# Kernel optimization log

Hardware: AMD Instinct MI355X
Metric: run time of the kernel (lower is better)

Reference implementation:

```python
import jax, jax.numpy as jnp
import numpy as np

N, K, C = 2, 512, 256
IMG = 1024.0
P = 7            # output_size
S = 2            # sampling_ratio
SCALES = (0.25, 0.125, 0.0625, 0.03125)
MIN_LEVEL, MAX_LEVEL = 2, 5
CANON_SIZE, CANON_LEVEL = 224.0, 4


def setup_inputs() -> dict:
    key = jax.random.key(0)
    ks = jax.random.split(key, 7)
    feats = {}
    for i, (hw, kk) in enumerate(zip((256, 128, 64, 32), ks[:4])):
        feats[f"feat{i + 2}"] = jax.random.normal(kk, (N, C, hw, hw), dtype=jnp.float32)
    # boxes: centers uniform in image, sizes log-uniform in [32, 512] px -> spans all levels
    cxy = jax.random.uniform(ks[4], (N, K, 2), minval=0.0, maxval=IMG)
    wh = 32.0 * jnp.exp2(jax.random.uniform(ks[5], (N, K, 2), minval=0.0, maxval=4.0))
    x1y1 = jnp.clip(cxy - wh / 2, 0.0, IMG)
    x2y2 = jnp.clip(cxy + wh / 2, 0.0, IMG)
    boxes = jnp.concatenate([x1y1, x2y2], axis=-1).astype(jnp.float32)  # [N,K,4] xyxy
    feats["boxes"] = boxes
    return feats


def _roi_align_level(feat, boxes, batch_idx, scale):
    """ROIAlignV2 (aligned=True). feat [N,C,H,W], boxes [M,4] xyxy in image coords."""
    Nf, Cf, H, W = feat.shape
    M = boxes.shape[0]
    b = boxes * scale - 0.5  # aligned=True shift
    x1, y1, x2, y2 = b[:, 0], b[:, 1], b[:, 2], b[:, 3]
    bin_h = (y2 - y1) / P
    bin_w = (x2 - x1) / P
    # combined bin+sample grid: coord = start + ((i + 0.5)/S) * bin, i in [0, P*S)
    g = (jnp.arange(P * S, dtype=feat.dtype) + 0.5) / S  # [PS]
    y = y1[:, None] + g[None, :] * bin_h[:, None]  # [M, PS]
    x = x1[:, None] + g[None, :] * bin_w[:, None]  # [M, PS]

    def prep(c, size):
        valid = (c >= -1.0) & (c <= size)
        c = jnp.maximum(c, 0.0)
        lo = jnp.minimum(jnp.floor(c).astype(jnp.int32), size - 1)
        hi = jnp.minimum(lo + 1, size - 1)
        frac = c - lo.astype(c.dtype)  # harmless if >1 when lo==hi==size-1
        return lo, hi, frac, valid

    yl, yh, fy, vy = prep(y, H)
    xl, xh, fx, vx = prep(x, W)
    bi = batch_idx[:, None, None]

    def gather(yy, xx):
        # -> [M, PS, PS, C]
        return feat[bi, :, yy[:, :, None], xx[:, None, :]]

    fy_ = fy[:, :, None, None]
    fx_ = fx[:, None, :, None]
    v = ((1 - fy_) * ((1 - fx_) * gather(yl, xl) + fx_ * gather(yl, xh))
         + fy_ * ((1 - fx_) * gather(yh, xl) + fx_ * gather(yh, xh)))
    mask = (vy[:, :, None] & vx[:, None, :])[..., None]
    v = jnp.where(mask, v, jnp.zeros((), feat.dtype))
    out = v.reshape(M, P, S, P, S, Cf).mean(axis=(2, 4))  # avg over sampling grid
    return out.transpose(0, 3, 1, 2)  # [M, C, P, P]


def reference(feat2, feat3, feat4, feat5, boxes):
    feats = [feat2, feat3, feat4, feat5]
    flat = boxes.reshape(-1, 4)  # [M,4], concat over images
    batch_idx = jnp.repeat(jnp.arange(N, dtype=jnp.int32), K)
    # assign_boxes_to_levels
    area = (flat[:, 2] - flat[:, 0]) * (flat[:, 3] - flat[:, 1])
    sizes = jnp.sqrt(area)
    lvl = jnp.floor(CANON_LEVEL + jnp.log2(sizes / CANON_SIZE + 1e-8))
    lvl = jnp.clip(lvl, MIN_LEVEL, MAX_LEVEL).astype(jnp.int32) - MIN_LEVEL  # [M] in 0..3
    out = jnp.zeros((flat.shape[0], C, P, P), dtype=feat2.dtype)
    for l, (feat, scale) in enumerate(zip(feats, SCALES)):
        o = _roi_align_level(feat, flat, batch_idx, scale)
        out = jnp.where((lvl == l)[:, None, None, None], o, out)
    return out
```

## Files before the change

kernel.cpp:

```cpp
#include <hip/hip_runtime.h>
#include <hip/hip_fp16.h>
#include <math.h>
#include <stdint.h>

#define NBATCH 2
#define KBOX   512
#define NBOX   (NBATCH*KBOX)
#define CCH    256
#define NBIN   49
#define NCH    4
#define BPB    (CCH/NCH)
#define COUT   (CCH*NBIN)
#define WCAP   1280
#define HDRN   32
#define TAPN   (12*NBIN)

typedef const uint32_t __attribute__((address_space(1)))* gas_u32p;
typedef uint32_t       __attribute__((address_space(3)))* las_u32p;

__global__ __launch_bounds__(64) void box_prep_kernel(
    const float* __restrict__ boxes, int* __restrict__ hdr, uint32_t* __restrict__ taps)
{
    const int m    = blockIdx.x;
    const int lane = threadIdx.x;

    __shared__ float    s_fy[14], s_fx[14];
    __shared__ int      s_slo[14], s_shi[14], s_xr[14];
    __shared__ int      s_vy[14], s_vx[14];
    __shared__ int      s_wsp4;
    __shared__ uint16_t s_roff[28];

    const float x1 = boxes[m*4+0];
    const float y1 = boxes[m*4+1];
    const float x2 = boxes[m*4+2];
    const float y2 = boxes[m*4+3];

    const float area = (x2 - x1) * (y2 - y1);
    const float size = sqrtf(area);
    float lvlf = floorf(4.0f + log2f(size / 224.0f + 1e-8f));
    lvlf = fminf(fmaxf(lvlf, 2.0f), 5.0f);
    const int lvl = (int)lvlf - 2;

    const int   H     = 256 >> lvl;
    const float scale = 0.25f / (float)(1 << lvl);
    const float Hf    = (float)H;

    const float bx1 = x1 * scale - 0.5f;
    const float by1 = y1 * scale - 0.5f;
    const float bin_w = (x2 * scale - 0.5f - bx1) / 7.0f;
    const float bin_h = (y2 * scale - 0.5f - by1) / 7.0f;

    if (lane == 0) {
        int xls[14];
        #pragma unroll 1
        for (int i = 0; i < 14; ++i) {
            const float gx = ((float)i + 0.5f) * 0.5f;
            const float xx = bx1 + gx * bin_w;
            s_vx[i] = (xx >= -1.0f) && (xx <= Hf);
            const float xc = fmaxf(xx, 0.0f);
            const int xl = min((int)floorf(xc), H - 1);
            const int xh = min(xl + 1, H - 1);
            float fx = xc - (float)xl;
            if (xh == xl) fx = 0.0f;
            s_fx[i] = fx;
            xls[i] = xl;
        }
        const int wx0a = xls[0] & ~3;
        const int xh13 = min(xls[13] + 1, H - 1);
        const int wsp4 = ((xh13 - wx0a + 1 + 3) >> 2) << 2;
        s_wsp4 = wsp4;
        #pragma unroll 1
        for (int i = 0; i < 14; ++i) s_xr[i] = xls[i] - wx0a;

        unsigned long long bm[4] = {0ull, 0ull, 0ull, 0ull};
        int yls[14], yhs[14];
        #pragma unroll 1
        for (int j = 0; j < 14; ++j) {
            const float gy = ((float)j + 0.5f) * 0.5f;
            const float yy = by1 + gy * bin_h;
            s_vy[j] = (yy >= -1.0f) && (yy <= Hf);
            const float yc = fmaxf(yy, 0.0f);
            const int yl = min((int)floorf(yc), H - 1);
            const int yh = min(yl + 1, H - 1);
            s_fy[j] = yc - (float)yl;
            yls[j] = yl; yhs[j] = yh;
            bm[yl >> 6] |= 1ull << (yl & 63);
            bm[yh >> 6] |= 1ull << (yh & 63);
        }
        int cum[4];
        cum[0] = 0;
        cum[1] = cum[0] + (int)__popcll(bm[0]);
        cum[2] = cum[1] + (int)__popcll(bm[1]);
        cum[3] = cum[2] + (int)__popcll(bm[2]);
        const int nr = cum[3] + (int)__popcll(bm[3]);
        #pragma unroll 1
        for (int j = 0; j < 14; ++j) {
            const int yl = yls[j], yh = yhs[j];
            s_slo[j] = cum[yl >> 6] + (int)__popcll(bm[yl >> 6] & ((1ull << (yl & 63)) - 1ull));
            s_shi[j] = cum[yh >> 6] + (int)__popcll(bm[yh >> 6] & ((1ull << (yh & 63)) - 1ull));
        }
        int slot = 0;
        #pragma unroll 1
        for (int w = 0; w < 4; ++w) {
            unsigned long long t = bm[w];
            while (t) {
                const int b = __builtin_ctzll(t);
                t &= t - 1ull;
                s_roff[slot++] = (uint16_t)(((w << 6) + b) * H + wx0a);
            }
        }
        #pragma unroll 1
        for (int r = slot; r < 28; ++r) s_roff[r] = s_roff[slot - 1];

        int* h = hdr + m * HDRN;
        const int qpr = wsp4 >> 2;
        const int nq  = nr * qpr;
        h[0] = lvl;
        h[1] = H;
        h[2] = H * H;
        h[3] = qpr;
        h[4] = nq;
        h[5] = __float_as_int(1.0f / (float)qpr);
        h[6] = nq << 2;
        h[7] = 0;
        uint32_t* hw = (uint32_t*)(h + 8);
        #pragma unroll 1
        for (int k = 0; k < 14; ++k)
            hw[k] = (uint32_t)s_roff[2*k] | ((uint32_t)s_roff[2*k+1] << 16);
    }
    __syncthreads();

    if (lane < NBIN) {
        const int py = lane / 7;
        const int px = lane - py * 7;
        const uint32_t base = (uint32_t)m * TAPN;
        __half2* th = (__half2*)taps;
        const int wsp4 = s_wsp4;

        #pragma unroll
        for (int s = 0; s < 4; ++s) {
            const int j = 2*py + (s >> 1);
            const int i = 2*px + (s & 1);
            const float fy = s_fy[j];
            const float fx = s_fx[i];
            const float vm = (s_vy[j] && s_vx[i]) ? 0.25f : 0.0f;
            const float wyl = (1.0f - fy) * vm;
            const float wyh = fy * vm;

            const uint32_t olo = (uint32_t)(s_slo[j] * wsp4 + s_xr[i]);
            const uint32_t ohi = (uint32_t)(s_shi[j] * wsp4 + s_xr[i]);

            taps[base + s*NBIN + lane] = olo | (ohi << 16);
            th  [base + (4+s)*NBIN + lane] = __floats2half2_rn(wyl*(1.0f-fx), wyh*(1.0f-fx));
            th  [base + (8+s)*NBIN + lane] = __floats2half2_rn(wyl*fx,        wyh*fx);
        }
    }
}

__global__ __launch_bounds__(256, 8) void roi_align_kernel(
    const float* __restrict__ f2, const float* __restrict__ f3,
    const float* __restrict__ f4, const float* __restrict__ f5,
    const int* __restrict__ hdr, const uint32_t* __restrict__ taps,
    float* __restrict__ out)
{
    const int bid  = blockIdx.x;
    const int m    = bid >> 6;
    const int cg   = bid & 63;
    const int tid  = threadIdx.x;
    const int lane = tid & 63;
    const int wid  = tid >> 6;
    const int b    = m >> 9;

    __shared__ float win[NCH * WCAP];

    const int* h = hdr + m * HDRN;
    const int   lvl = h[0];
    const int   HH  = h[2];
    const int   qpr = h[3];
    const int   nq  = h[4];
    const float rq  = __int_as_float(h[5]);
    const int   nq4 = h[6];

    const uint32_t roww = ((const uint32_t*)(h + 8))[min(lane, 13)];

    const float* fptr = (lvl == 0) ? f2 : (lvl == 1) ? f3 : (lvl == 2) ? f4 : f5;
    const int c = cg * NCH + wid;
    const float* plane = fptr + ((size_t)(b * CCH + c)) * HH;
    float* wbase = win + wid * WCAP;

    const int niter = (nq + 63) >> 6;
    for (int it = 0; it < niter; ++it) {
        const int iq  = (it << 6) + lane;
        const int iqc = min(iq, nq - 1);
        const int slot = (int)(((float)iqc + 0.5f) * rq);
        const int cq   = iqc - slot * qpr;
        const uint32_t w2 = (uint32_t)__shfl((int)roww, slot >> 1, 64);
        const int roff = (slot & 1) ? (int)(w2 >> 16) : (int)(w2 & 0xffffu);
        if (iq < nq) {
            __builtin_amdgcn_global_load_lds(
                (gas_u32p)(const void*)(plane + roff + (cq << 2)),
                (las_u32p)(void*)(&wbase[it << 8]),
                16, 0, 0);
        }
    }
    if (lane == 0) wbase[nq4] = 0.0f;

    const int l = (lane < NBIN) ? lane : NBIN - 1;
    const uint32_t* tb = taps + (uint32_t)m * TAPN;
    const __half2*  th = (const __half2*)tb;

    uint32_t po[4];
    __half2  wl[4], wh[4];
    #pragma unroll
    for (int s = 0; s < 4; ++s) po[s] = tb[s*NBIN + l];
    #pragma unroll
    for (int s = 0; s < 4; ++s) wl[s] = th[(4+s)*NBIN + l];
    #pragma unroll
    for (int s = 0; s < 4; ++s) wh[s] = th[(8+s)*NBIN + l];

    asm volatile("s_waitcnt vmcnt(0) lgkmcnt(0)" ::: "memory");
    __builtin_amdgcn_sched_barrier(0);

    float acc = 0.0f;
    #pragma unroll
    for (int s = 0; s < 4; ++s) {
        const int olo = (int)(po[s] & 0xffffu);
        const int ohi = (int)(po[s] >> 16);
        const float2 a  = __half22float2(wl[s]);
        const float2 bw = __half22float2(wh[s]);
        acc += a.x * wbase[olo] + bw.x * wbase[olo + 1];
        acc += a.y * wbase[ohi] + bw.y * wbase[ohi + 1];
    }

    if (lane < NBIN) {
        __builtin_nontemporal_store(
            acc, out + (size_t)m * COUT + (size_t)c * NBIN + lane);
    }
}

extern "C" void kernel_launch(void* const* d_in, const int* in_sizes, int n_in,
                              void* d_out, int out_size, void* d_ws, size_t ws_size,
                              hipStream_t stream) {
    const float* f2    = (const float*)d_in[0];
    const float* f3    = (const float*)d_in[1];
    const float* f4    = (const float*)d_in[2];
    const float* f5    = (const float*)d_in[3];
    const float* boxes = (const float*)d_in[4];
    float* outp = (float*)d_out;

    int*      hdr  = (int*)d_ws;
    uint32_t* taps = (uint32_t*)d_ws + NBOX * HDRN;

    box_prep_kernel<<<dim3(NBOX), dim3(64), 0, stream>>>(boxes, hdr, taps);
    roi_align_kernel<<<dim3(NBOX * BPB), dim3(256), 0, stream>>>(
        f2, f3, f4, f5, hdr, taps, outp);
}
```

Baseline: 110.3 us.

## Process two channels per wave and interleave tap records for vector loads

Each wave now handles two channels, so the tap offsets and weights it loads and the index math it does are shared across both channels. The grid shrinks to half the blocks. Tap data is stored interleaved per bin so each lane fetches its 12 words with three 16-byte vector loads instead of twelve strided scalar loads. The LDS window per channel is reduced to 1024 floats, which keeps total shared memory similar, and the occupancy hint drops to 5. The costs are lower parallelism, more registers per thread, and a risk of overflowing the window if a box needs more than 1024 floats.

```diff
diff --git a/kernel.cpp b/kernel.cpp
--- a/kernel.cpp
+++ b/kernel.cpp
@@ -8,10 +8,12 @@
 #define NBOX   (NBATCH*KBOX)
 #define CCH    256
 #define NBIN   49
-#define NCH    4
-#define BPB    (CCH/NCH)
+#define CPW    2
+#define WAVES  4
+#define CHB    (CPW*WAVES)
+#define BPB    (CCH/CHB)
 #define COUT   (CCH*NBIN)
-#define WCAP   1280
+#define WCAP   1024
 #define HDRN   32
 #define TAPN   (12*NBIN)
 
@@ -133,8 +135,7 @@
     if (lane < NBIN) {
         const int py = lane / 7;
         const int px = lane - py * 7;
-        const uint32_t base = (uint32_t)m * TAPN;
-        __half2* th = (__half2*)taps;
+        uint32_t* tp = taps + ((uint32_t)m * NBIN + lane) * 12u;
         const int wsp4 = s_wsp4;
 
         #pragma unroll
@@ -150,28 +151,31 @@
             const uint32_t olo = (uint32_t)(s_slo[j] * wsp4 + s_xr[i]);
             const uint32_t ohi = (uint32_t)(s_shi[j] * wsp4 + s_xr[i]);
 
-            taps[base + s*NBIN + lane] = olo | (ohi << 16);
-            th  [base + (4+s)*NBIN + lane] = __floats2half2_rn(wyl*(1.0f-fx), wyh*(1.0f-fx));
-            th  [base + (8+s)*NBIN + lane] = __floats2half2_rn(wyl*fx,        wyh*fx);
+            const __half2 wlo2 = __floats2half2_rn(wyl*(1.0f-fx), wyh*(1.0f-fx));
+            const __half2 whi2 = __floats2half2_rn(wyl*fx,        wyh*fx);
+
+            tp[s]     = olo | (ohi << 16);
+            tp[4 + s] = *reinterpret_cast<const uint32_t*>(&wlo2);
+            tp[8 + s] = *reinterpret_cast<const uint32_t*>(&whi2);
         }
     }
 }
 
-__global__ __launch_bounds__(256, 8) void roi_align_kernel(
+__global__ __launch_bounds__(256, 5) void roi_align_kernel(
     const float* __restrict__ f2, const float* __restrict__ f3,
     const float* __restrict__ f4, const float* __restrict__ f5,
     const int* __restrict__ hdr, const uint32_t* __restrict__ taps,
     float* __restrict__ out)
 {
     const int bid  = blockIdx.x;
-    const int m    = bid >> 6;
-    const int cg   = bid & 63;
+    const int m    = bid >> 5;
+    const int cg   = bid & 31;
     const int tid  = threadIdx.x;
     const int lane = tid & 63;
     const int wid  = tid >> 6;
     const int b    = m >> 9;
 
-    __shared__ float win[NCH * WCAP];
+    __shared__ float win[WAVES * CPW * WCAP];
 
     const int* h = hdr + m * HDRN;
     const int   lvl = h[0];
@@ -184,9 +188,11 @@
     const uint32_t roww = ((const uint32_t*)(h + 8))[min(lane, 13)];
 
     const float* fptr = (lvl == 0) ? f2 : (lvl == 1) ? f3 : (lvl == 2) ? f4 : f5;
-    const int c = cg * NCH + wid;
-    const float* plane = fptr + ((size_t)(b * CCH + c)) * HH;
-    float* wbase = win + wid * WCAP;
+    const int c0 = cg * CHB + wid * CPW;
+    const float* plane0 = fptr + ((size_t)(b * CCH + c0)) * HH;
+    const float* plane1 = plane0 + HH;
+    float* wb0 = win + (wid * CPW) * WCAP;
+    float* wb1 = wb0 + WCAP;
 
     const int niter = (nq + 63) >> 6;
     for (int it = 0; it < niter; ++it) {
@@ -195,46 +201,48 @@
         const int slot = (int)(((float)iqc + 0.5f) * rq);
         const int cq   = iqc - slot * qpr;
         const uint32_t w2 = (uint32_t)__shfl((int)roww, slot >> 1, 64);
-        const int roff = (slot & 1) ? (int)(w2 >> 16) : (int)(w2 & 0xffffu);
+        const int roff = (((slot & 1) ? (int)(w2 >> 16) : (int)(w2 & 0xffffu))) + (cq << 2);
         if (iq < nq) {
             __builtin_amdgcn_global_load_lds(
-                (gas_u32p)(const void*)(plane + roff + (cq << 2)),
-                (las_u32p)(void*)(&wbase[it << 8]),
-                16, 0, 0);
-        }
-    }
-    if (lane == 0) wbase[nq4] = 0.0f;
+                (gas_u32p)(const void*)(plane0 + roff),
+                (las_u32p)(void*)(&wb0[it << 8]), 16, 0, 0);
+            __builtin_amdgcn_global_load_lds(
+                (gas_u32p)(const void*)(plane1 + roff),
+                (las_u32p)(void*)(&wb1[it << 8]), 16, 0, 0);
+        }
+    }
+    if (lane < CPW) win[(wid * CPW + lane) * WCAP + nq4] = 0.0f;
 
     const int l = (lane < NBIN) ? lane : NBIN - 1;
-    const uint32_t* tb = taps + (uint32_t)m * TAPN;
-    const __half2*  th = (const __half2*)tb;
-
-    uint32_t po[4];
-    __half2  wl[4], wh[4];
-    #pragma unroll
-    for (int s = 0; s < 4; ++s) po[s] = tb[s*NBIN + l];
-    #pragma unroll
-    for (int s = 0; s < 4; ++s) wl[s] = th[(4+s)*NBIN + l];
-    #pragma unroll
-    for (int s = 0; s < 4; ++s) wh[s] = th[(8+s)*NBIN + l];
+    const uint32_t* tp = taps + ((uint32_t)m * NBIN + l) * 12u;
+    const uint4 tpo = *reinterpret_cast<const uint4*>(tp);
+    const uint4 twl = *reinterpret_cast<const uint4*>(tp + 4);
+    const uint4 twh = *reinterpret_cast<const uint4*>(tp + 8);
 
     asm volatile("s_waitcnt vmcnt(0) lgkmcnt(0)" ::: "memory");
     __builtin_amdgcn_sched_barrier(0);
 
-    float acc = 0.0f;
+    const uint32_t pos[4] = {tpo.x, tpo.y, tpo.z, tpo.w};
+    const uint32_t wls[4] = {twl.x, twl.y, twl.z, twl.w};
+    const uint32_t whs[4] = {twh.x, twh.y, twh.z, twh.w};
+
+    float acc0 = 0.0f, acc1 = 0.0f;
     #pragma unroll
     for (int s = 0; s < 4; ++s) {
-        const int olo = (int)(po[s] & 0xffffu);
-        const int ohi = (int)(po[s] >> 16);
-        const float2 a  = __half22float2(wl[s]);
-        const float2 bw = __half22float2(wh[s]);
-        acc += a.x * wbase[olo] + bw.x * wbase[olo + 1];
-        acc += a.y * wbase[ohi] + bw.y * wbase[ohi + 1];
+        const int olo = (int)(pos[s] & 0xffffu);
+        const int ohi = (int)(pos[s] >> 16);
+        const float2 a  = __half22float2(*reinterpret_cast<const __half2*>(&wls[s]));
+        const float2 bw = __half22float2(*reinterpret_cast<const __half2*>(&whs[s]));
+        acc0 += a.x * wb0[olo] + bw.x * wb0[olo + 1];
+        acc0 += a.y * wb0[ohi] + bw.y * wb0[ohi + 1];
+        acc1 += a.x * wb1[olo] + bw.x * wb1[olo + 1];
+        acc1 += a.y * wb1[ohi] + bw.y * wb1[ohi + 1];
     }
 
     if (lane < NBIN) {
-        __builtin_nontemporal_store(
-            acc, out + (size_t)m * COUT + (size_t)c * NBIN + lane);
+        float* outp = out + (size_t)m * COUT + (size_t)c0 * NBIN + lane;
+        __builtin_nontemporal_store(acc0, outp);
+        __builtin_nontemporal_store(acc1, outp + NBIN);
     }
 }
 
```

Result: slower. 113.4 us (+2.8%).
